# Performance work log

Hardware: AMD Instinct MI355X
Metric: run time of the kernel (lower is better)

## Reference

```python
import jax, jax.numpy as jnp
import numpy as np

EPS = 1e-12  # F.normalize default eps


def _l2_normalize(x):
    # F.normalize(x, p=2) normalizes over dim=1 (channels) by default
    n = jnp.sqrt(jnp.sum(x * x, axis=1, keepdims=True))
    return x / jnp.maximum(n, EPS)


def _cost_volume(left, right, num_disp):
    # left, right: (N, C, H, W)
    l = _l2_normalize(left)
    r = _l2_normalize(right)
    # dot[n,h,x,y] = sum_c l[n,c,h,x] * r[n,c,h,y]   -> (N, H, W, W)
    dot = jnp.einsum('nchx,nchy->nhxy', l, r)
    W = left.shape[-1]
    x = jnp.arange(W)                                   # (W,)
    j = jnp.arange(num_disp)                            # (D,)
    # torch.diagonal(offset=-j) + F.pad((j,0)) picks dot[..., x, x-j] with zeros for x<j
    idx = jnp.clip(x[None, :] - j[:, None], 0, W - 1)   # (D, W)
    g = dot[:, :, x[None, :], idx]                      # (N, H, D, W)
    valid = (x[None, :] >= j[:, None])                  # (D, W)
    g = jnp.where(valid[None, None, :, :], g, jnp.zeros((), dtype=g.dtype))
    return jnp.transpose(g, (0, 2, 1, 3))               # (N, D, H, W)


def setup_inputs() -> dict:
    key = jax.random.key(0)
    ks = jax.random.split(key, 6)
    shapes = [(2, 32, 256, 512), (2, 64, 128, 256), (2, 96, 64, 128)]
    inp = {}
    for i, s in enumerate(shapes):
        inp[f'left{i}'] = jax.random.normal(ks[2 * i], s, dtype=jnp.float32)
        inp[f'right{i}'] = jax.random.normal(ks[2 * i + 1], s, dtype=jnp.float32)
    inp['max_disparity'] = 128
    return inp


def reference(left0, right0, left1, right1, left2, right2, max_disparity):
    lefts = [left0, left1, left2]
    rights = [right0, right1, right2]
    md = min(int(max_disparity), lefts[0].shape[-1])
    cost_volumes = []
    for i, (l, r) in enumerate(zip(lefts, rights)):
        cost_volumes.append(_cost_volume(l, r, md // (2 ** i)))
    return tuple(cost_volumes)
```

## Files before the change

### kernel.cpp

```cpp
#include <hip/hip_runtime.h>

typedef __attribute__((ext_vector_type(8))) short bf16x8;
typedef __attribute__((ext_vector_type(4))) float f32x4;
typedef __attribute__((ext_vector_type(4))) _Float16 f16x4;

static __device__ __forceinline__ unsigned short f32_to_bf16(float f) {
    unsigned int x = __float_as_uint(f);
    x += 0x7fffu + ((x >> 16) & 1u);
    return (unsigned short)(x >> 16);
}

static constexpr int SMEM_BYTES = 38400;

template<int C, int H, int W, int D, int TX, int NT>
__device__ __forceinline__
void cv_body(const int bx, const float* __restrict__ Lp, const float* __restrict__ Rp,
             float* __restrict__ out, char* smem)
{
    constexpr int RS = TX + D;
    constexpr int AS = C + 8;
    constexpr int KC = C / 32;
    constexpr int NW = NT / 64;
    static_assert(NW == TX / 16, "one wave per 16-wide x-strip");
    static_assert(TX + RS <= NT, "staging: one column per thread");
    static_assert(TX == 64, "obuf swizzle assumes 128B rows; wave-aligned branch split");
    static_assert(RS * AS * 2 + TX * AS * 2 + (RS + TX) * 4 + D * TX * 2 <= SMEM_BYTES, "lds");

    unsigned short* Abf = (unsigned short*)smem;
    unsigned short* Bbf = Abf + RS * AS;
    float* invA = (float*)(Bbf + TX * AS);
    float* invB = invA + RS;
    char*  obuf = (char*)(invB + TX);

    const int tid = threadIdx.x;
    constexpr int NXB = W / TX;
    const int xb = bx % NXB;
    const int h  = (bx / NXB) % H;
    const int n  = bx / (NXB * H);
    const int X0 = xb * TX;

    const size_t CH = (size_t)H * W;
    const float* Lb = Lp + ((size_t)n * C * H + h) * W;
    const float* Rb = Rp + ((size_t)n * C * H + h) * W;

    const int col = tid;
    if (col < TX + RS) {
        const float* src; unsigned short* dst; int g; bool zero;
        if (col < TX) { g = X0 + col;            src = Lb; dst = Bbf + col * AS;        zero = false; }
        else          { g = X0 - D + (col - TX); src = Rb; dst = Abf + (col - TX) * AS; zero = g < 0; }
        float ssq = 0.f;
        if (!zero) {
            #pragma unroll
            for (int c0 = 0; c0 < C; c0 += 8) {
                float v[8];
                #pragma unroll
                for (int k = 0; k < 8; ++k) v[k] = src[(size_t)(c0 + k) * CH + g];
                union { unsigned short us[8]; uint4 q; } p;
                #pragma unroll
                for (int k = 0; k < 8; ++k) { ssq += v[k] * v[k]; p.us[k] = f32_to_bf16(v[k]); }
                *(uint4*)&dst[c0] = p.q;
            }
        } else {
            const uint4 z = {0u, 0u, 0u, 0u};
            #pragma unroll
            for (int c0 = 0; c0 < C; c0 += 8) *(uint4*)&dst[c0] = z;
        }
        const float inv = 1.0f / fmaxf(sqrtf(ssq), 1e-12f);
        if (col < TX) invB[col] = inv; else invA[col - TX] = inv;
    }
    __syncthreads();

    const int wave = tid >> 6, lane = tid & 63;
    const int colc = lane & 15, quad = lane >> 4;

    bf16x8 bfr[KC];
    #pragma unroll
    for (int kc = 0; kc < KC; ++kc)
        bfr[kc] = *(const bf16x8*)&Bbf[(wave * 16 + colc) * AS + kc * 32 + quad * 8];

    const int xl = wave * 16 + colc;
    const float sB = invB[xl];

    #pragma unroll
    for (int t = 0; t <= D / 16; ++t) {
        const int yt = wave + t;
        f32x4 acc = {0.f, 0.f, 0.f, 0.f};
        #pragma unroll
        for (int kc = 0; kc < KC; ++kc) {
            const bf16x8 a = *(const bf16x8*)&Abf[(yt * 16 + colc) * AS + kc * 32 + quad * 8];
            acc = __builtin_amdgcn_mfma_f32_16x16x32_bf16(a, bfr[kc], acc, 0, 0, 0);
        }
        const int yb = yt * 16 + quad * 4;
        const int jb = D + xl - yb;
        #pragma unroll
        for (int r = 0; r < 4; ++r) {
            const int j = jb - r;
            if (j >= 0 && j < D) {
                const float val = acc[r] * sB * invA[yb + r];
                *(_Float16*)(obuf + (((j * TX + xl) * 2) ^ ((j & 7) << 4))) = (_Float16)val;
            }
        }
    }
    __syncthreads();

    constexpr int NIT = D * TX / 4 / NT;
    float* orow = out + ((size_t)n * D) * CH + (size_t)h * W + X0;
    #pragma unroll
    for (int it = 0; it < NIT; ++it) {
        const int idx = it * NT + tid;
        const int j = idx >> 4, xo = idx & 15;
        const f16x4 hv = *(const f16x4*)(obuf + (((j * TX + xo * 4) * 2) ^ ((j & 7) << 4)));
        float4 o;
        o.x = (float)hv.x; o.y = (float)hv.y; o.z = (float)hv.z; o.w = (float)hv.w;
        *(float4*)&orow[(size_t)j * CH + xo * 4] = o;
    }
}

constexpr int G0 = 2 * 256 * (512 / 64);
constexpr int G1 = 2 * 128 * (256 / 64);
constexpr int G2 = 2 * 64  * (128 / 64);

static __device__ __forceinline__ int xcd_swz(int b, int nwg) {
    return (b & 7) * (nwg >> 3) + (b >> 3);
}

__global__ __launch_bounds__(256, 4)
void fused_cv(const float* __restrict__ l0, const float* __restrict__ r0, float* __restrict__ o0,
              const float* __restrict__ l1, const float* __restrict__ r1, float* __restrict__ o1,
              const float* __restrict__ l2, const float* __restrict__ r2, float* __restrict__ o2)
{
    __shared__ __align__(16) char smem[SMEM_BYTES];
    const int bid = blockIdx.x;
    if (bid < G0)
        cv_body<32, 256, 512, 128, 64, 256>(xcd_swz(bid, G0), l0, r0, o0, smem);
    else if (bid < G0 + G1)
        cv_body<64, 128, 256,  64, 64, 256>(xcd_swz(bid - G0, G1), l1, r1, o1, smem);
    else
        cv_body<96,  64, 128,  32, 64, 256>(xcd_swz(bid - G0 - G1, G2), l2, r2, o2, smem);
}

extern "C" void kernel_launch(void* const* d_in, const int* in_sizes, int n_in,
                              void* d_out, int out_size, void* d_ws, size_t ws_size,
                              hipStream_t stream) {
    (void)in_sizes; (void)n_in; (void)d_ws; (void)ws_size; (void)out_size;
    const float* l0 = (const float*)d_in[0];
    const float* r0 = (const float*)d_in[1];
    const float* l1 = (const float*)d_in[2];
    const float* r1 = (const float*)d_in[3];
    const float* l2 = (const float*)d_in[4];
    const float* r2 = (const float*)d_in[5];

    float* o0 = (float*)d_out;
    float* o1 = o0 + (size_t)2 * 128 * 256 * 512;
    float* o2 = o1 + (size_t)2 * 64 * 128 * 256;

    fused_cv<<<G0 + G1 + G2, 256, 0, stream>>>(l0, r0, o0, l1, r1, o1, l2, r2, o2);
}
```

Baseline: 254.8 us.

## Alias output buffer with staging LDS, split tiles across waves, narrow TX for small levels

The fp16 output staging buffer now reuses the LDS region that held the bf16 A/B tiles, with an extra barrier between the MFMA phase and the scatter. This shrinks LDS per block so more blocks fit per CU, and launch bounds are raised to 5. Levels 1 and 2 use a 32-wide x tile, with multiple waves per 16-column strip splitting the diagonal tiles, which doubles their block counts. Output stores become nontemporal. The trade-offs are more accumulator registers held across the barrier and more redundant R-column staging for the narrower tiles.

New measurement: 255.6 us. No clear change (+0.3%).

```diff
diff --git a/kernel.cpp b/kernel.cpp
--- a/kernel.cpp
+++ b/kernel.cpp
@@ -10,27 +10,33 @@
     return (unsigned short)(x >> 16);
 }
 
-static constexpr int SMEM_BYTES = 38400;
+static constexpr int SMEM_BYTES = 21504;
 
-template<int C, int H, int W, int D, int TX, int NT>
+template<int C, int H, int W, int D, int TX>
 __device__ __forceinline__
 void cv_body(const int bx, const float* __restrict__ Lp, const float* __restrict__ Rp,
              float* __restrict__ out, char* smem)
 {
+    constexpr int NT = 256;
     constexpr int RS = TX + D;
     constexpr int AS = C + 8;
     constexpr int KC = C / 32;
-    constexpr int NW = NT / 64;
-    static_assert(NW == TX / 16, "one wave per 16-wide x-strip");
+    constexpr int NSTRIP = TX / 16;
+    constexpr int WPS = (NT / 64) / NSTRIP;
+    constexpr int NTT = D / 16 + 1;
+    constexpr int TPW = (NTT + WPS - 1) / WPS;
+    constexpr int STAGE_B = (RS + TX) * AS * 2;
+    constexpr int OBUF_B  = D * TX * 2;
+    constexpr int UNION_B = STAGE_B > OBUF_B ? STAGE_B : OBUF_B;
+    static_assert(UNION_B + (RS + TX) * 4 <= SMEM_BYTES, "lds budget");
     static_assert(TX + RS <= NT, "staging: one column per thread");
-    static_assert(TX == 64, "obuf swizzle assumes 128B rows; wave-aligned branch split");
-    static_assert(RS * AS * 2 + TX * AS * 2 + (RS + TX) * 4 + D * TX * 2 <= SMEM_BYTES, "lds");
+    static_assert(WPS * 64 * NSTRIP == NT, "wave partition");
 
     unsigned short* Abf = (unsigned short*)smem;
     unsigned short* Bbf = Abf + RS * AS;
-    float* invA = (float*)(Bbf + TX * AS);
+    char*  obuf = smem;
+    float* invA = (float*)(smem + UNION_B);
     float* invB = invA + RS;
-    char*  obuf = (char*)(invB + TX);
 
     const int tid = threadIdx.x;
     constexpr int NXB = W / TX;
@@ -72,59 +78,76 @@
 
     const int wave = tid >> 6, lane = tid & 63;
     const int colc = lane & 15, quad = lane >> 4;
+    const int strip = wave % NSTRIP;
+    const int tslc  = wave / NSTRIP;
 
     bf16x8 bfr[KC];
     #pragma unroll
     for (int kc = 0; kc < KC; ++kc)
-        bfr[kc] = *(const bf16x8*)&Bbf[(wave * 16 + colc) * AS + kc * 32 + quad * 8];
+        bfr[kc] = *(const bf16x8*)&Bbf[(strip * 16 + colc) * AS + kc * 32 + quad * 8];
 
-    const int xl = wave * 16 + colc;
+    const int xl = strip * 16 + colc;
     const float sB = invB[xl];
 
+    f32x4 acc[TPW];
     #pragma unroll
-    for (int t = 0; t <= D / 16; ++t) {
-        const int yt = wave + t;
-        f32x4 acc = {0.f, 0.f, 0.f, 0.f};
-        #pragma unroll
-        for (int kc = 0; kc < KC; ++kc) {
-            const bf16x8 a = *(const bf16x8*)&Abf[(yt * 16 + colc) * AS + kc * 32 + quad * 8];
-            acc = __builtin_amdgcn_mfma_f32_16x16x32_bf16(a, bfr[kc], acc, 0, 0, 0);
-        }
-        const int yb = yt * 16 + quad * 4;
-        const int jb = D + xl - yb;
-        #pragma unroll
-        for (int r = 0; r < 4; ++r) {
-            const int j = jb - r;
-            if (j >= 0 && j < D) {
-                const float val = acc[r] * sB * invA[yb + r];
-                *(_Float16*)(obuf + (((j * TX + xl) * 2) ^ ((j & 7) << 4))) = (_Float16)val;
+    for (int tt = 0; tt < TPW; ++tt) {
+        acc[tt] = {0.f, 0.f, 0.f, 0.f};
+        const int t = tslc + tt * WPS;
+        if (t < NTT) {
+            const int yt = strip + t;
+            #pragma unroll
+            for (int kc = 0; kc < KC; ++kc) {
+                const bf16x8 a =
+                    *(const bf16x8*)&Abf[(yt * 16 + colc) * AS + kc * 32 + quad * 8];
+                acc[tt] = __builtin_amdgcn_mfma_f32_16x16x32_bf16(a, bfr[kc], acc[tt], 0, 0, 0);
             }
         }
     }
     __syncthreads();
 
+    #pragma unroll
+    for (int tt = 0; tt < TPW; ++tt) {
+        const int t = tslc + tt * WPS;
+        if (t < NTT) {
+            const int yt = strip + t;
+            const int yb = yt * 16 + quad * 4;
+            const int jb = D + xl - yb;
+            #pragma unroll
+            for (int r = 0; r < 4; ++r) {
+                const int j = jb - r;
+                if (j >= 0 && j < D) {
+                    const float val = acc[tt][r] * sB * invA[yb + r];
+                    *(_Float16*)(obuf + (((j * TX + xl) * 2) ^ ((j & 7) << 4))) = (_Float16)val;
+                }
+            }
+        }
+    }
+    __syncthreads();
+
+    constexpr int JV = TX / 4;
     constexpr int NIT = D * TX / 4 / NT;
     float* orow = out + ((size_t)n * D) * CH + (size_t)h * W + X0;
     #pragma unroll
     for (int it = 0; it < NIT; ++it) {
         const int idx = it * NT + tid;
-        const int j = idx >> 4, xo = idx & 15;
+        const int j = idx / JV, xo = idx % JV;
         const f16x4 hv = *(const f16x4*)(obuf + (((j * TX + xo * 4) * 2) ^ ((j & 7) << 4)));
-        float4 o;
+        f32x4 o;
         o.x = (float)hv.x; o.y = (float)hv.y; o.z = (float)hv.z; o.w = (float)hv.w;
-        *(float4*)&orow[(size_t)j * CH + xo * 4] = o;
+        __builtin_nontemporal_store(o, (f32x4*)&orow[(size_t)j * CH + xo * 4]);
     }
 }
 
 constexpr int G0 = 2 * 256 * (512 / 64);
-constexpr int G1 = 2 * 128 * (256 / 64);
-constexpr int G2 = 2 * 64  * (128 / 64);
+constexpr int G1 = 2 * 128 * (256 / 32);
+constexpr int G2 = 2 * 64  * (128 / 32);
 
 static __device__ __forceinline__ int xcd_swz(int b, int nwg) {
     return (b & 7) * (nwg >> 3) + (b >> 3);
 }
 
-__global__ __launch_bounds__(256, 4)
+__global__ __launch_bounds__(256, 5)
 void fused_cv(const float* __restrict__ l0, const float* __restrict__ r0, float* __restrict__ o0,
               const float* __restrict__ l1, const float* __restrict__ r1, float* __restrict__ o1,
               const float* __restrict__ l2, const float* __restrict__ r2, float* __restrict__ o2)
@@ -132,11 +155,11 @@
     __shared__ __align__(16) char smem[SMEM_BYTES];
     const int bid = blockIdx.x;
     if (bid < G0)
-        cv_body<32, 256, 512, 128, 64, 256>(xcd_swz(bid, G0), l0, r0, o0, smem);
+        cv_body<32, 256, 512, 128, 64>(xcd_swz(bid, G0), l0, r0, o0, smem);
     else if (bid < G0 + G1)
-        cv_body<64, 128, 256,  64, 64, 256>(xcd_swz(bid - G0, G1), l1, r1, o1, smem);
+        cv_body<64, 128, 256,  64, 32>(xcd_swz(bid - G0, G1), l1, r1, o1, smem);
     else
-        cv_body<96,  64, 128,  32, 64, 256>(xcd_swz(bid - G0 - G1, G2), l2, r2, o2, smem);
+        cv_body<96,  64, 128,  32, 32>(xcd_swz(bid - G0 - G1, G2), l2, r2, o2, smem);
 }
 
 extern "C" void kernel_launch(void* const* d_in, const int* in_sizes, int n_in,
```
